# Kernel tuning notes

Hardware: AMD Instinct MI355X
Metric: run time of the kernel (lower is better)

## Reference

```python
import jax, jax.numpy as jnp
import numpy as np

HID = 128
CIN = 256


def setup_inputs() -> dict:
    key = jax.random.key(0)
    k1, k2, k3, k4, k5, k6 = jax.random.split(key, 6)
    b, c, h, w = 32, CIN, 32, 32
    left_features = jax.random.normal(k1, (b, c, h, w), dtype=jnp.float32)
    right_features = jax.random.normal(k2, (b, c, h, w), dtype=jnp.float32)
    # 1x1 conv weights (stored as [out_ch, in_ch]) + biases
    Wq = jax.random.normal(k3, (HID, CIN), dtype=jnp.float32) * (1.0 / np.sqrt(CIN))
    bq = jax.random.normal(k4, (HID,), dtype=jnp.float32) * 0.01
    Wk = jax.random.normal(k5, (HID, CIN), dtype=jnp.float32) * (1.0 / np.sqrt(CIN))
    bk = jax.random.normal(k6, (HID,), dtype=jnp.float32) * 0.01
    return {"left_features": left_features, "right_features": right_features,
            "Wq": Wq, "bq": bq, "Wk": Wk, "bk": bk, "vis_CA": 0}


def reference(left_features, right_features, Wq, bq, Wk, bk, vis_CA):
    b, c, h, w = right_features.shape
    # 1x1 convs = per-pixel linear projections
    Q = jnp.einsum('oc,bchw->bohw', Wq, left_features) + bq[None, :, None, None]   # [b,HID,h,w]
    K = jnp.einsum('oc,bchw->bohw', Wk, right_features) + bk[None, :, None, None]  # [b,HID,h,w]
    V = right_features.reshape(b, c, h * w)                                        # [b,c,hw]
    # global cross-attention over all spatial locations
    attn = jnp.einsum('bcij,bckl->bijkl', Q, K).reshape(b, h, w, h * w)            # [b,h,w,hw]
    attn = jax.nn.softmax(attn, axis=3)
    attended = jnp.einsum('bijp,bcp->bcij', attn, V)                               # [b,c,h,w]
    # rearrange([left, attended], 'two b c h w -> b (two c) h w')
    return jnp.concatenate([left_features, attended], axis=1)                      # [b,2c,h,w]
```

## Files before the change

### kernel.cpp

```cpp
#include <hip/hip_runtime.h>
#include <stdint.h>
#include <stddef.h>

#define NPIX  1024
#define DHID  128
#define CIN   256

typedef _Float16 f16;
typedef __attribute__((ext_vector_type(4))) _Float16 f16x4;
typedef __attribute__((ext_vector_type(8))) _Float16 f16x8;
typedef __attribute__((ext_vector_type(4))) float f32x4;
typedef __attribute__((ext_vector_type(16))) float f32x16;

#define MFMA16(a,b,c) __builtin_amdgcn_mfma_f32_16x16x32_f16((a),(b),(c),0,0,0)
#define MFMA32(a,b,c) __builtin_amdgcn_mfma_f32_32x32x16_f16((a),(b),(c),0,0,0)

typedef const __attribute__((address_space(1))) uint32_t GU32;
typedef __attribute__((address_space(3))) uint32_t LU32;

__device__ __forceinline__ void gll16(const void* g, void* l) {
  __builtin_amdgcn_global_load_lds((GU32*)g, (LU32*)l, 16, 0, 0);
}

__global__ void wprep_kernel(const float* __restrict__ Wq, const float* __restrict__ Wk,
                             f16* __restrict__ Whq, f16* __restrict__ Whk) {
  int i = blockIdx.x * 256 + threadIdx.x;
  if (i < DHID * CIN) { Whq[i] = (f16)Wq[i]; Whk[i] = (f16)Wk[i]; }
}

__global__ __launch_bounds__(256) void proj_kernel(
    const float* __restrict__ Xl, const float* __restrict__ Xr,
    const f16* __restrict__ Whq, const f16* __restrict__ Whk,
    const float* __restrict__ bq, const float* __restrict__ bk,
    f16* __restrict__ QT, f16* __restrict__ KT,
    float* __restrict__ out, f16* __restrict__ Vb)
{
  __shared__ char smem[64 * 264 * 2];
  f16* sXT = (f16*)smem;
  f16* sO  = (f16*)smem;

  const int tid = threadIdx.x;
  const int w = tid >> 6, lane = tid & 63, g = lane >> 4, r16 = lane & 15;
  const int p0 = blockIdx.x * 64, b = blockIdx.y;
  const bool isK = (blockIdx.z != 0);

  const float* X = (isK ? Xr : Xl) + (size_t)b * CIN * NPIX;
  const f16* Wh = isK ? Whk : Whq;
  const float* bias = isK ? bk : bq;
  f16* QKT = (isK ? KT : QT) + (size_t)b * NPIX * DHID;

  const int cl = tid >> 4;
  const int p4 = (tid & 15) * 4;
  const int csw = (tid & 3) << 3;
#pragma unroll
  for (int i = 0; i < 16; ++i) {
    int c = cl + 16 * i;
    f32x4 v = *(const f32x4*)(X + (size_t)c * NPIX + p0 + p4);
    if (!isK) *(f32x4*)(out + ((size_t)b * 2 * CIN + c) * NPIX + p0 + p4) = v;
    f16x4 hv = {(f16)v.x, (f16)v.y, (f16)v.z, (f16)v.w};
    if (isK) *(f16x4*)(Vb + ((size_t)b * CIN + c) * NPIX + p0 + p4) = hv;
    int cs = c ^ csw;
#pragma unroll
    for (int j = 0; j < 4; ++j) sXT[(p4 + j) * 264 + cs] = hv[j];
  }
  __syncthreads();

  const int prow = 16 * w + r16;
  const int swzp = ((r16 >> 2) & 3) << 3;
  f16x8 xb[8];
#pragma unroll
  for (int kc = 0; kc < 8; ++kc)
    xb[kc] = *(const f16x8*)(sXT + prow * 264 + ((kc * 32 + 8 * g) ^ swzp));

  f32x4 acc[8];
#pragma unroll
  for (int i = 0; i < 8; ++i)
#pragma unroll
    for (int j = 0; j < 4; ++j) acc[i][j] = 0.f;

#pragma unroll
  for (int kc = 0; kc < 8; ++kc)
#pragma unroll
    for (int dt = 0; dt < 8; ++dt) {
      f16x8 wa = *(const f16x8*)(Wh + (size_t)(dt * 16 + r16) * CIN + kc * 32 + 8 * g);
      acc[dt] = MFMA16(wa, xb[kc], acc[dt]);
    }

  __syncthreads();

#pragma unroll
  for (int dt = 0; dt < 8; ++dt) {
    f16x4 hv;
#pragma unroll
    for (int r = 0; r < 4; ++r) hv[r] = (f16)(acc[dt][r] + bias[dt * 16 + 4 * g + r]);
    *(f16x4*)(&sO[(16 * w + r16) * 136 + dt * 16 + 4 * g]) = hv;
  }
  __syncthreads();
  const int pr = tid >> 2, dseg = (tid & 3) * 32;
#pragma unroll
  for (int i = 0; i < 4; ++i) {
    f16x8 row = *(const f16x8*)(&sO[pr * 136 + dseg + 8 * i]);
    *(f16x8*)(QKT + (size_t)(p0 + pr) * DHID + dseg + 8 * i) = row;
  }
}

__global__ __launch_bounds__(256) void attn_kernel(
    const f16* __restrict__ QT, const f16* __restrict__ KT,
    const f16* __restrict__ Vb, float* __restrict__ out)
{
  __shared__ f16 sK[128 * 128];
  __shared__ f16 sP[32 * 128];
  __shared__ float sM[4][32], sL[4][32];

  const int tid = threadIdx.x;
  const int w = tid >> 6, lane = tid & 63;
  const int h = lane >> 5, l31 = lane & 31;
  const int x = blockIdx.x;
  const int b = (x & 7) * 4 + ((x >> 3) & 3);
  const int q0 = (x >> 5) * 32;

  const f16* QTb = QT + ((size_t)b * NPIX + q0 + l31) * DHID;
  const f16* KTb = KT + (size_t)b * NPIX * DHID;
  const f16* vBb = Vb + (size_t)b * CIN * NPIX;

  f16x8 qf[8];
#pragma unroll
  for (int kt = 0; kt < 8; ++kt) qf[kt] = *(const f16x8*)(QTb + 16 * kt + 8 * h);

#define STAGE(tt)                                                              \
  {                                                                            \
    _Pragma("unroll")                                                          \
    for (int i = 0; i < 8; ++i) {                                              \
      int chunk = tid + 256 * i;                                               \
      int row = chunk >> 4, cc = chunk & 15;                                   \
      gll16(KTb + (size_t)((tt) * 128 + row) * DHID + ((cc ^ (row & 7)) * 8),  \
            &sK[chunk * 8]);                                                   \
    }                                                                          \
  }

  f32x16 oacc[2];
#pragma unroll
  for (int i = 0; i < 2; ++i)
#pragma unroll
    for (int j = 0; j < 16; ++j) oacc[i][j] = 0.f;
  float mrun = -3.0e38f, lrun = 0.f;

  const int swzq = (l31 & 7) << 4;
  char* sPq = (char*)sP + l31 * 256;

  STAGE(0);
  __syncthreads();

  for (int t = 0; t < 8; ++t) {
    const int r = 32 * w + l31;
    const int swzr = (l31 & 7) << 4;
    const char* sKc = (const char*)sK;
    f32x16 s;
#pragma unroll
    for (int j = 0; j < 16; ++j) s[j] = 0.f;
#pragma unroll
    for (int kt = 0; kt < 8; ++kt) {
      f16x8 kf = *(const f16x8*)(sKc + r * 256 + ((32 * kt + 16 * h) ^ swzr));
      s = MFMA32(kf, qf[kt], s);
    }

    float m_w = s[0];
#pragma unroll
    for (int j = 1; j < 16; ++j) m_w = fmaxf(m_w, s[j]);
    m_w = fmaxf(m_w, __shfl_xor(m_w, 32));
    if (lane < 32) sM[w][lane] = m_w;
    __syncthreads();

    if (t < 7) STAGE(t + 1);

    float m_tile = fmaxf(fmaxf(sM[0][l31], sM[1][l31]),
                         fmaxf(sM[2][l31], sM[3][l31]));
    if (__any(m_tile > mrun + 8.f)) {
      float mnew = fmaxf(mrun, m_tile);
      float sc = __expf(mrun - mnew);
      lrun *= sc; mrun = mnew;
#pragma unroll
      for (int i = 0; i < 2; ++i)
#pragma unroll
        for (int j = 0; j < 16; ++j) oacc[i][j] *= sc;
    }

    float psum = 0.f;
#pragma unroll
    for (int r4 = 0; r4 < 4; ++r4) {
      f16x4 p4v;
#pragma unroll
      for (int j = 0; j < 4; ++j) {
        float pe = __expf(s[4 * r4 + j] - mrun);
        psum += pe; p4v[j] = (f16)pe;
      }
      *(f16x4*)(sPq + (((64 * w + 16 * r4 + 8 * h)) ^ swzq)) = p4v;
    }
    psum += __shfl_xor(psum, 32);
    if (lane < 32) sL[w][lane] = psum;
    __syncthreads();
    lrun += sL[0][l31] + sL[1][l31] + sL[2][l31] + sL[3][l31];

    f16x8 pf[8];
#pragma unroll
    for (int km = 0; km < 8; ++km)
      pf[km] = *(const f16x8*)(sPq + ((32 * km + 16 * h) ^ swzq));
#pragma unroll
    for (int ct = 0; ct < 2; ++ct) {
      const f16* vrow = vBb + (size_t)(64 * w + 32 * ct + l31) * NPIX + 128 * t + 8 * h;
#pragma unroll
      for (int km = 0; km < 8; ++km) {
        f16x8 vf = *(const f16x8*)(vrow + 16 * km);
        oacc[ct] = MFMA32(vf, pf[km], oacc[ct]);
      }
    }
    __syncthreads();
  }

  float inv = 1.f / lrun;
  float* ob = out + ((size_t)b * 2 * CIN + CIN) * NPIX + q0 + l31;
#pragma unroll
  for (int ct = 0; ct < 2; ++ct)
#pragma unroll
    for (int rg = 0; rg < 16; ++rg) {
      int c = 64 * w + 32 * ct + (rg & 3) + 8 * (rg >> 2) + 4 * h;
      ob[(size_t)c * NPIX] = oacc[ct][rg] * inv;
    }
}

extern "C" void kernel_launch(void* const* d_in, const int* in_sizes, int n_in,
                              void* d_out, int out_size, void* d_ws, size_t ws_size,
                              hipStream_t stream) {
  const float* left  = (const float*)d_in[0];
  const float* right = (const float*)d_in[1];
  const float* Wq    = (const float*)d_in[2];
  const float* bq    = (const float*)d_in[3];
  const float* Wk    = (const float*)d_in[4];
  const float* bk    = (const float*)d_in[5];
  float* out = (float*)d_out;
  char* ws = (char*)d_ws;

  f16* Whq = (f16*)(ws);
  f16* Whk = (f16*)(ws + 65536);
  size_t off = 131072;
  const size_t QSZ = (size_t)32 * NPIX * DHID * sizeof(f16);
  f16* QT = (f16*)(ws + off); off += QSZ;
  f16* KT = (f16*)(ws + off); off += QSZ;
  f16* Vb = (f16*)(ws + off); off += (size_t)32 * CIN * NPIX * sizeof(f16);
  (void)ws_size; (void)in_sizes; (void)n_in; (void)out_size;

  wprep_kernel<<<128, 256, 0, stream>>>(Wq, Wk, Whq, Whk);

  dim3 pgrid(16, 32, 2);
  proj_kernel<<<pgrid, 256, 0, stream>>>(left, right, Whq, Whk, bq, bk,
                                         QT, KT, out, Vb);

  attn_kernel<<<1024, 256, 0, stream>>>(QT, KT, Vb, out);
}
```

Before: 236.6 us.

## Restructure attention with 128-query blocks, double-buffered K/V in LDS, register P

The attention kernel now runs 512-thread blocks covering 128 queries, with 8 waves split into 4 query groups and 2 channel halves. K and V tiles of 64 keys are double-buffered in LDS through async global-to-LDS loads, so V is no longer read straight from global memory and K/V reuse across queries goes up. Each wave owns its full query softmax, which removes the cross-wave max/sum exchange through shared memory. P is packed to fp16 in registers and rearranged by lane shuffles instead of a round trip through LDS. The projection kernel batches its loads ahead of the stores and gets an occupancy hint; in exchange the grid shrinks to 256 blocks and register and LDS pressure rise.

```diff
diff --git a/kernel.cpp b/kernel.cpp
--- a/kernel.cpp
+++ b/kernel.cpp
@@ -9,6 +9,7 @@
 typedef _Float16 f16;
 typedef __attribute__((ext_vector_type(4))) _Float16 f16x4;
 typedef __attribute__((ext_vector_type(8))) _Float16 f16x8;
+typedef __attribute__((ext_vector_type(2))) __fp16 fp16x2_raw;
 typedef __attribute__((ext_vector_type(4))) float f32x4;
 typedef __attribute__((ext_vector_type(16))) float f32x16;
 
@@ -20,6 +21,11 @@
 
 __device__ __forceinline__ void gll16(const void* g, void* l) {
   __builtin_amdgcn_global_load_lds((GU32*)g, (LU32*)l, 16, 0, 0);
+}
+
+__device__ __forceinline__ uint32_t pkh(float a, float b) {
+  fp16x2_raw p = __builtin_amdgcn_cvt_pkrtz(a, b);
+  return __builtin_bit_cast(uint32_t, p);
 }
 
 __global__ void wprep_kernel(const float* __restrict__ Wq, const float* __restrict__ Wk,
@@ -28,7 +34,7 @@
   if (i < DHID * CIN) { Whq[i] = (f16)Wq[i]; Whk[i] = (f16)Wk[i]; }
 }
 
-__global__ __launch_bounds__(256) void proj_kernel(
+__global__ __launch_bounds__(256, 3) void proj_kernel(
     const float* __restrict__ Xl, const float* __restrict__ Xr,
     const f16* __restrict__ Whq, const f16* __restrict__ Whk,
     const float* __restrict__ bq, const float* __restrict__ bk,
@@ -52,16 +58,26 @@
   const int cl = tid >> 4;
   const int p4 = (tid & 15) * 4;
   const int csw = (tid & 3) << 3;
-#pragma unroll
-  for (int i = 0; i < 16; ++i) {
-    int c = cl + 16 * i;
-    f32x4 v = *(const f32x4*)(X + (size_t)c * NPIX + p0 + p4);
-    if (!isK) *(f32x4*)(out + ((size_t)b * 2 * CIN + c) * NPIX + p0 + p4) = v;
-    f16x4 hv = {(f16)v.x, (f16)v.y, (f16)v.z, (f16)v.w};
-    if (isK) *(f16x4*)(Vb + ((size_t)b * CIN + c) * NPIX + p0 + p4) = hv;
-    int cs = c ^ csw;
-#pragma unroll
-    for (int j = 0; j < 4; ++j) sXT[(p4 + j) * 264 + cs] = hv[j];
+
+#pragma unroll
+  for (int half = 0; half < 2; ++half) {
+    f32x4 ld[8];
+#pragma unroll
+    for (int i = 0; i < 8; ++i) {
+      int c = cl + 16 * (8 * half + i);
+      ld[i] = *(const f32x4*)(X + (size_t)c * NPIX + p0 + p4);
+    }
+#pragma unroll
+    for (int i = 0; i < 8; ++i) {
+      int c = cl + 16 * (8 * half + i);
+      f32x4 v = ld[i];
+      if (!isK) *(f32x4*)(out + ((size_t)b * 2 * CIN + c) * NPIX + p0 + p4) = v;
+      f16x4 hv = {(f16)v.x, (f16)v.y, (f16)v.z, (f16)v.w};
+      if (isK) *(f16x4*)(Vb + ((size_t)b * CIN + c) * NPIX + p0 + p4) = hv;
+      int cs = c ^ csw;
+#pragma unroll
+      for (int j = 0; j < 4; ++j) sXT[(p4 + j) * 264 + cs] = hv[j];
+    }
   }
   __syncthreads();
 
@@ -104,20 +120,20 @@
   }
 }
 
-__global__ __launch_bounds__(256) void attn_kernel(
+__global__ __launch_bounds__(512, 2) void attn_kernel(
     const f16* __restrict__ QT, const f16* __restrict__ KT,
     const f16* __restrict__ Vb, float* __restrict__ out)
 {
-  __shared__ f16 sK[128 * 128];
-  __shared__ f16 sP[32 * 128];
-  __shared__ float sM[4][32], sL[4][32];
+  __shared__ f16 sK[2][64 * 128];
+  __shared__ f16 sV[2][256 * 64];
 
   const int tid = threadIdx.x;
   const int w = tid >> 6, lane = tid & 63;
   const int h = lane >> 5, l31 = lane & 31;
+  const int qw = w & 3, ch = w >> 2;
   const int x = blockIdx.x;
-  const int b = (x & 7) * 4 + ((x >> 3) & 3);
-  const int q0 = (x >> 5) * 32;
+  const int b = x & 31;
+  const int q0 = (x >> 5) * 128 + qw * 32;
 
   const f16* QTb = QT + ((size_t)b * NPIX + q0 + l31) * DHID;
   const f16* KTb = KT + (size_t)b * NPIX * DHID;
@@ -127,103 +143,122 @@
 #pragma unroll
   for (int kt = 0; kt < 8; ++kt) qf[kt] = *(const f16x8*)(QTb + 16 * kt + 8 * h);
 
-#define STAGE(tt)                                                              \
+#define STAGE_K(tt, bf)                                                        \
   {                                                                            \
     _Pragma("unroll")                                                          \
-    for (int i = 0; i < 8; ++i) {                                              \
-      int chunk = tid + 256 * i;                                               \
-      int row = chunk >> 4, cc = chunk & 15;                                   \
-      gll16(KTb + (size_t)((tt) * 128 + row) * DHID + ((cc ^ (row & 7)) * 8),  \
-            &sK[chunk * 8]);                                                   \
+    for (int i_ = 0; i_ < 2; ++i_) {                                           \
+      int ck_ = tid + 512 * i_;                                                \
+      int rw_ = ck_ >> 4, cc_ = ck_ & 15;                                      \
+      gll16(KTb + (size_t)((tt) * 64 + rw_) * DHID + ((cc_ ^ (rw_ & 7)) * 8),  \
+            &sK[bf][ck_ * 8]);                                                 \
     }                                                                          \
   }
-
-  f32x16 oacc[2];
-#pragma unroll
-  for (int i = 0; i < 2; ++i)
+#define STAGE_V(tt, bf)                                                        \
+  {                                                                            \
+    _Pragma("unroll")                                                          \
+    for (int i_ = 0; i_ < 4; ++i_) {                                           \
+      int ck_ = tid + 512 * i_;                                                \
+      int rw_ = ck_ >> 3, cc_ = ck_ & 7;                                       \
+      gll16(vBb + (size_t)rw_ * NPIX + (tt) * 64 + ((cc_ ^ (rw_ & 7)) * 8),    \
+            &sV[bf][ck_ * 8]);                                                 \
+    }                                                                          \
+  }
+
+  f32x16 oacc[4];
+#pragma unroll
+  for (int i = 0; i < 4; ++i)
 #pragma unroll
     for (int j = 0; j < 16; ++j) oacc[i][j] = 0.f;
   float mrun = -3.0e38f, lrun = 0.f;
 
-  const int swzq = (l31 & 7) << 4;
-  char* sPq = (char*)sP + l31 * 256;
-
-  STAGE(0);
-  __syncthreads();
-
-  for (int t = 0; t < 8; ++t) {
-    const int r = 32 * w + l31;
-    const int swzr = (l31 & 7) << 4;
-    const char* sKc = (const char*)sK;
-    f32x16 s;
-#pragma unroll
-    for (int j = 0; j < 16; ++j) s[j] = 0.f;
+  union PF { uint32_t u[4]; f16x8 v; };
+
+  STAGE_K(0, 0);
+  STAGE_V(0, 0);
+  __syncthreads();
+
+  for (int t = 0; t < 16; ++t) {
+    const int cur = t & 1;
+    if (t < 15) { STAGE_K(t + 1, cur ^ 1); STAGE_V(t + 1, cur ^ 1); }
+
+    f32x16 s0, s1;
+#pragma unroll
+    for (int j = 0; j < 16; ++j) { s0[j] = 0.f; s1[j] = 0.f; }
+    const char* kb = (const char*)&sK[cur][0];
+    const int sw8 = l31 & 7;
 #pragma unroll
     for (int kt = 0; kt < 8; ++kt) {
-      f16x8 kf = *(const f16x8*)(sKc + r * 256 + ((32 * kt + 16 * h) ^ swzr));
-      s = MFMA32(kf, qf[kt], s);
-    }
-
-    float m_w = s[0];
-#pragma unroll
-    for (int j = 1; j < 16; ++j) m_w = fmaxf(m_w, s[j]);
-    m_w = fmaxf(m_w, __shfl_xor(m_w, 32));
-    if (lane < 32) sM[w][lane] = m_w;
+      f16x8 k0 = *(const f16x8*)(kb + l31 * 256 + (((2 * kt + h) ^ sw8) << 4));
+      f16x8 k1 = *(const f16x8*)(kb + (32 + l31) * 256 + (((2 * kt + h) ^ sw8) << 4));
+      s0 = MFMA32(k0, qf[kt], s0);
+      s1 = MFMA32(k1, qf[kt], s1);
+    }
+
+    float pmax = s0[0];
+#pragma unroll
+    for (int j = 0; j < 16; ++j) { pmax = fmaxf(pmax, s0[j]); pmax = fmaxf(pmax, s1[j]); }
+    pmax = fmaxf(pmax, __shfl_xor(pmax, 32));
+    if (__any(pmax > mrun + 8.f)) {
+      float mnew = fmaxf(mrun, pmax);
+      float sc = __expf(mrun - mnew);
+      mrun = mnew; lrun *= sc;
+#pragma unroll
+      for (int i = 0; i < 4; ++i)
+#pragma unroll
+        for (int j = 0; j < 16; ++j) oacc[i][j] *= sc;
+    }
+    float psum = 0.f;
+#pragma unroll
+    for (int j = 0; j < 16; ++j) {
+      s0[j] = __expf(s0[j] - mrun); psum += s0[j];
+      s1[j] = __expf(s1[j] - mrun); psum += s1[j];
+    }
+    psum += __shfl_xor(psum, 32);
+    lrun += psum;
+
+    uint32_t u0[8], u1[8];
+#pragma unroll
+    for (int qd = 0; qd < 4; ++qd) {
+      u0[qd]     = pkh(s0[4 * qd], s0[4 * qd + 1]);
+      u1[qd]     = pkh(s0[4 * qd + 2], s0[4 * qd + 3]);
+      u0[4 + qd] = pkh(s1[4 * qd], s1[4 * qd + 1]);
+      u1[4 + qd] = pkh(s1[4 * qd + 2], s1[4 * qd + 3]);
+    }
+    PF pf[4];
+#pragma unroll
+    for (int pk = 0; pk < 4; ++pk) {
+      uint32_t A = u0[2 * pk], B = u0[2 * pk + 1];
+      uint32_t C = u1[2 * pk], D = u1[2 * pk + 1];
+      uint32_t sA = (uint32_t)__shfl_xor((int)A, 32);
+      uint32_t sB = (uint32_t)__shfl_xor((int)B, 32);
+      uint32_t sC = (uint32_t)__shfl_xor((int)C, 32);
+      uint32_t sD = (uint32_t)__shfl_xor((int)D, 32);
+      pf[pk].u[0] = h ? sB : A;
+      pf[pk].u[1] = h ? sD : C;
+      pf[pk].u[2] = h ? B : sA;
+      pf[pk].u[3] = h ? D : sC;
+    }
+
+    const char* vbp = (const char*)&sV[cur][0];
+#pragma unroll
+    for (int ct = 0; ct < 4; ++ct) {
+      int row = 128 * ch + 32 * ct + l31;
+#pragma unroll
+      for (int pk = 0; pk < 4; ++pk) {
+        f16x8 vf = *(const f16x8*)(vbp + row * 128 + (((2 * pk + h) ^ sw8) << 4));
+        oacc[ct] = MFMA32(vf, pf[pk].v, oacc[ct]);
+      }
+    }
     __syncthreads();
-
-    if (t < 7) STAGE(t + 1);
-
-    float m_tile = fmaxf(fmaxf(sM[0][l31], sM[1][l31]),
-                         fmaxf(sM[2][l31], sM[3][l31]));
-    if (__any(m_tile > mrun + 8.f)) {
-      float mnew = fmaxf(mrun, m_tile);
-      float sc = __expf(mrun - mnew);
-      lrun *= sc; mrun = mnew;
-#pragma unroll
-      for (int i = 0; i < 2; ++i)
-#pragma unroll
-        for (int j = 0; j < 16; ++j) oacc[i][j] *= sc;
-    }
-
-    float psum = 0.f;
-#pragma unroll
-    for (int r4 = 0; r4 < 4; ++r4) {
-      f16x4 p4v;
-#pragma unroll
-      for (int j = 0; j < 4; ++j) {
-        float pe = __expf(s[4 * r4 + j] - mrun);
-        psum += pe; p4v[j] = (f16)pe;
-      }
-      *(f16x4*)(sPq + (((64 * w + 16 * r4 + 8 * h)) ^ swzq)) = p4v;
-    }
-    psum += __shfl_xor(psum, 32);
-    if (lane < 32) sL[w][lane] = psum;
-    __syncthreads();
-    lrun += sL[0][l31] + sL[1][l31] + sL[2][l31] + sL[3][l31];
-
-    f16x8 pf[8];
-#pragma unroll
-    for (int km = 0; km < 8; ++km)
-      pf[km] = *(const f16x8*)(sPq + ((32 * km + 16 * h) ^ swzq));
-#pragma unroll
-    for (int ct = 0; ct < 2; ++ct) {
-      const f16* vrow = vBb + (size_t)(64 * w + 32 * ct + l31) * NPIX + 128 * t + 8 * h;
-#pragma unroll
-      for (int km = 0; km < 8; ++km) {
-        f16x8 vf = *(const f16x8*)(vrow + 16 * km);
-        oacc[ct] = MFMA32(vf, pf[km], oacc[ct]);
-      }
-    }
-    __syncthreads();
   }
 
   float inv = 1.f / lrun;
-  float* ob = out + ((size_t)b * 2 * CIN + CIN) * NPIX + q0 + l31;
-#pragma unroll
-  for (int ct = 0; ct < 2; ++ct)
+  float* ob = out + ((size_t)b * 2 * CIN + CIN + 128 * ch) * NPIX + q0 + l31;
+#pragma unroll
+  for (int ct = 0; ct < 4; ++ct)
 #pragma unroll
     for (int rg = 0; rg < 16; ++rg) {
-      int c = 64 * w + 32 * ct + (rg & 3) + 8 * (rg >> 2) + 4 * h;
+      int c = 32 * ct + (rg & 3) + 8 * (rg >> 2) + 4 * h;
       ob[(size_t)c * NPIX] = oacc[ct][rg] * inv;
     }
 }
@@ -255,5 +290,5 @@
   proj_kernel<<<pgrid, 256, 0, stream>>>(left, right, Whq, Whk, bq, bk,
                                          QT, KT, out, Vb);
 
-  attn_kernel<<<1024, 256, 0, stream>>>(QT, KT, Vb, out);
-}
+  attn_kernel<<<256, 512, 0, stream>>>(QT, KT, Vb, out);
+}
```

After: 200.1 us. -15.4%, faster.
